# Performance work log

Measured on AMD Instinct MI355X. Metric: run time of the kernel, lower is better.

Reference implementation:

```python
import jax, jax.numpy as jnp
import numpy as np

N_EMBD = 768
HEAD_SIZE = 64
B, T = 8, 4096


def setup_inputs() -> dict:
    key = jax.random.key(0)
    ks = jax.random.split(key, 7)
    s = 0.02  # small init scale for weights
    return {
        "x": jax.random.normal(ks[0], (B, T, N_EMBD), dtype=jnp.float32),
        "Wq": jax.random.normal(ks[1], (N_EMBD, HEAD_SIZE), dtype=jnp.float32) * s,
        "bq": jax.random.normal(ks[2], (HEAD_SIZE,), dtype=jnp.float32) * s,
        "Wk": jax.random.normal(ks[3], (N_EMBD, HEAD_SIZE), dtype=jnp.float32) * s,
        "bk": jax.random.normal(ks[4], (HEAD_SIZE,), dtype=jnp.float32) * s,
        "Wv": jax.random.normal(ks[5], (N_EMBD, HEAD_SIZE), dtype=jnp.float32) * s,
        "bv": jax.random.normal(ks[6], (HEAD_SIZE,), dtype=jnp.float32) * s,
    }


def reference(x, Wq, bq, Wk, bk, Wv, bv):
    # x: [B, T, C]; note: scale uses C = n_embd (input dim), per the original code.
    C = x.shape[-1]
    scale = jnp.asarray(C, x.dtype) ** -0.5
    q = x @ Wq + bq  # [B, T, H]
    k = x @ Wk + bk  # [B, T, H]
    v = x @ Wv + bv  # [B, T, H]
    wei = jnp.einsum("bqh,bkh->bqk", q, k) * scale  # [B, T, T]
    att = jax.nn.softmax(wei, axis=-1)
    # dropout p=0.0 (eval mode) -> identity
    out = jnp.einsum("bqk,bkh->bqh", att, v)  # [B, T, H]
    return out
```

## Files before the change

### kernel.cpp

```cpp
#include <hip/hip_runtime.h>
#include <stdint.h>

#define T_SEQ 4096
#define CEMB 768
#define HS 64

typedef __attribute__((ext_vector_type(8))) short bf16x8;
typedef __attribute__((ext_vector_type(16))) float f32x16;

__device__ __forceinline__ short bfru(float f) {
    uint32_t u = __builtin_bit_cast(uint32_t, f);
    return (short)((u + 0x8000u) >> 16);
}
__device__ __forceinline__ short bftr(float f) {
    return (short)(__builtin_bit_cast(uint32_t, f) >> 16);
}

#define QSCALE (0.036084391824351615f * 1.4426950408889634f)

__global__ __launch_bounds__(256) void prep_wt(const float* __restrict__ Wq,
                                               const float* __restrict__ Wk,
                                               const float* __restrict__ Wv,
                                               short* __restrict__ wtf) {
    const int p = blockIdx.x;
    const int ct = p / 48, kq = p % 48;
    const int tid = threadIdx.x;
    const int lane = tid & 63, jp = tid >> 6;
    const int l31 = lane & 31, lhi = lane >> 5;
    const int k = kq * 16 + lhi * 8 + jp * 2;
    const int nn = ct * 32 + l31;
    const float* W = nn < 64 ? Wq : (nn < 128 ? Wk : Wv);
    const int col = nn & 63;
    uint32_t lo = (uint16_t)bfru(W[k * 64 + col]);
    uint32_t hi = (uint16_t)bfru(W[(k + 1) * 64 + col]);
    *(uint32_t*)&wtf[(p * 64 + lane) * 8 + jp * 2] = lo | (hi << 16);
}

__global__ __launch_bounds__(256) void qkv_proj(const float* __restrict__ x,
        const float* __restrict__ bq, const float* __restrict__ bk, const float* __restrict__ bv,
        const short* __restrict__ wtf,
        short* __restrict__ qo, short* __restrict__ ko, short* __restrict__ vto) {
    __shared__ short S[64 * 72];

    const int tid  = threadIdx.x;
    const int wave = tid >> 6, lane = tid & 63;
    const int l31  = lane & 31, lhi = lane >> 5;
    const int rg   = wave & 1;
    const int ctb  = (wave >> 1) * 3;
    const int rowbase = blockIdx.x * 64;

    f32x16 acc[3];
    #pragma unroll
    for (int c = 0; c < 3; ++c) {
        const int ct = ctb + c, nn = ct * 32 + l31;
        const float bb = nn < 64 ? bq[nn] : (nn < 128 ? bk[nn - 64] : bv[nn - 128]);
        #pragma unroll
        for (int r = 0; r < 16; ++r) acc[c][r] = bb;
    }

    const int sr = tid >> 2, sseg = (tid & 3) * 16;
    for (int kt = 0; kt < 12; ++kt) {
        const float4* src = (const float4*)(x + (long)(rowbase + sr) * CEMB + kt * 64 + sseg);
        float4 f0 = src[0], f1 = src[1], f2 = src[2], f3 = src[3];
        bf16x8 w0, w1;
        w0[0]=bfru(f0.x); w0[1]=bfru(f0.y); w0[2]=bfru(f0.z); w0[3]=bfru(f0.w);
        w0[4]=bfru(f1.x); w0[5]=bfru(f1.y); w0[6]=bfru(f1.z); w0[7]=bfru(f1.w);
        w1[0]=bfru(f2.x); w1[1]=bfru(f2.y); w1[2]=bfru(f2.z); w1[3]=bfru(f2.w);
        w1[4]=bfru(f3.x); w1[5]=bfru(f3.y); w1[6]=bfru(f3.z); w1[7]=bfru(f3.w);
        *(bf16x8*)&S[sr * 72 + sseg]     = w0;
        *(bf16x8*)&S[sr * 72 + sseg + 8] = w1;
        __syncthreads();
        #pragma unroll
        for (int kc = 0; kc < 4; ++kc) {
            bf16x8 af = *(const bf16x8*)&S[(rg * 32 + l31) * 72 + kc * 16 + lhi * 8];
            #pragma unroll
            for (int c = 0; c < 3; ++c) {
                bf16x8 wf = *(const bf16x8*)&wtf[((ctb + c) * 48 + kt * 4 + kc) * 512 + lane * 8];
                acc[c] = __builtin_amdgcn_mfma_f32_32x32x16_bf16(af, wf, acc[c], 0, 0, 0);
            }
        }
        __syncthreads();
    }

    #pragma unroll
    for (int c = 0; c < 3; ++c) {
        const int ct = ctb + c;
        if (ct < 2) {
            #pragma unroll
            for (int r = 0; r < 16; ++r) {
                const int row = rg * 32 + (r & 3) + 8 * (r >> 2) + 4 * lhi;
                qo[(long)(rowbase + row) * HS + ct * 32 + l31] = bfru(acc[c][r] * QSCALE);
            }
        } else if (ct < 4) {
            #pragma unroll
            for (int r = 0; r < 16; ++r) {
                const int row = rg * 32 + (r & 3) + 8 * (r >> 2) + 4 * lhi;
                ko[(long)(rowbase + row) * HS + (ct - 2) * 32 + l31] = bfru(acc[c][r]);
            }
        } else {
            #pragma unroll
            for (int r = 0; r < 16; ++r) {
                const int row = rg * 32 + (r & 3) + 8 * (r >> 2) + 4 * lhi;
                S[((ct - 4) * 32 + l31) * 72 + row] = bfru(acc[c][r]);
            }
        }
    }
    __syncthreads();
    if (tid < 128) {
        const int vcol = tid >> 1, hh = tid & 1;
        const int b = rowbase >> 12, t0 = rowbase & 4095;
        short* dst = vto + ((long)b * HS + vcol) * T_SEQ + t0 + hh * 32;
        #pragma unroll
        for (int i = 0; i < 4; ++i)
            *(bf16x8*)(dst + i * 8) = *(const bf16x8*)&S[vcol * 72 + hh * 32 + i * 8];
    }
}

__global__ __launch_bounds__(256, 4) void attn(const short* __restrict__ qm,
        const short* __restrict__ km, const short* __restrict__ vtm,
        float* __restrict__ Op, float* __restrict__ lp, const int ks,
        float* __restrict__ outdirect) {
    __shared__ short Klds[64 * 72];
    __shared__ short Vlds[64 * 72];
    __shared__ short Plds[4][32 * 40];

    const int tid  = threadIdx.x;
    const int wave = tid >> 6, lane = tid & 63;
    const int l31  = lane & 31, lhi = lane >> 5;
    const int idx  = blockIdx.x;
    const int b = idx & 7, s = (idx >> 3) % ks, qt = idx / (8 * ks);
    const int slab = T_SEQ / ks, nkt = slab / 64;

    const short* qb = qm + ((long)b * T_SEQ + qt * 128) * HS;
    const short* kb = km + ((long)b * T_SEQ + s * slab) * HS;
    const short* vb = vtm + (long)b * HS * T_SEQ + s * slab;

    bf16x8 qf[4];
    #pragma unroll
    for (int kc = 0; kc < 4; ++kc)
        qf[kc] = *(const bf16x8*)&qb[(wave * 32 + l31) * HS + kc * 16 + lhi * 8];

    bf16x8 ones;
    #pragma unroll
    for (int j = 0; j < 8; ++j) ones[j] = (short)0x3F80;

    f32x16 oacc[2] = {};
    f32x16 lacc = {};
    short* pw = &Plds[wave][0];

    const int sr = tid >> 2, sc = (tid & 3) * 16;
    for (int kt = 0; kt < nkt; ++kt) {
        const int k0 = kt * 64;
        {   const short* p1 = &kb[(k0 + sr) * HS + sc];
            *(bf16x8*)&Klds[sr * 72 + sc]     = *(const bf16x8*)p1;
            *(bf16x8*)&Klds[sr * 72 + sc + 8] = *(const bf16x8*)(p1 + 8); }
        {   const short* p2 = &vb[sr * T_SEQ + k0 + sc];
            *(bf16x8*)&Vlds[sr * 72 + sc]     = *(const bf16x8*)p2;
            *(bf16x8*)&Vlds[sr * 72 + sc + 8] = *(const bf16x8*)(p2 + 8); }
        __syncthreads();

        #pragma unroll
        for (int ct = 0; ct < 2; ++ct) {
            f32x16 z = {};
            #pragma unroll
            for (int kc = 0; kc < 4; ++kc) {
                bf16x8 kf = *(const bf16x8*)&Klds[(ct * 32 + l31) * 72 + kc * 16 + lhi * 8];
                z = __builtin_amdgcn_mfma_f32_32x32x16_bf16(qf[kc], kf, z, 0, 0, 0);
            }
            #pragma unroll
            for (int r = 0; r < 16; ++r) {
                const int row = (r & 3) + 8 * (r >> 2) + 4 * lhi;
                pw[row * 40 + l31] = bftr(__builtin_amdgcn_exp2f(z[r]));
            }
            #pragma unroll
            for (int kc2 = 0; kc2 < 2; ++kc2) {
                bf16x8 pf = *(const bf16x8*)&pw[l31 * 40 + kc2 * 16 + lhi * 8];
                lacc = __builtin_amdgcn_mfma_f32_32x32x16_bf16(pf, ones, lacc, 0, 0, 0);
                #pragma unroll
                for (int ht = 0; ht < 2; ++ht) {
                    bf16x8 vf = *(const bf16x8*)&Vlds[(ht * 32 + l31) * 72 + ct * 32 + kc2 * 16 + lhi * 8];
                    oacc[ht] = __builtin_amdgcn_mfma_f32_32x32x16_bf16(pf, vf, oacc[ht], 0, 0, 0);
                }
            }
        }
        __syncthreads();
    }

    const long rowg = (long)b * T_SEQ + qt * 128 + wave * 32;
    if (outdirect) {
        float* ob = outdirect + rowg * HS;
        #pragma unroll
        for (int ht = 0; ht < 2; ++ht)
            #pragma unroll
            for (int r = 0; r < 16; ++r) {
                const int row = (r & 3) + 8 * (r >> 2) + 4 * lhi;
                ob[row * HS + ht * 32 + l31] = oacc[ht][r] / lacc[r];
            }
    } else {
        float* op = Op + ((long)s * 32768 + rowg) * HS;
        #pragma unroll
        for (int ht = 0; ht < 2; ++ht)
            #pragma unroll
            for (int r = 0; r < 16; ++r) {
                const int row = (r & 3) + 8 * (r >> 2) + 4 * lhi;
                op[row * HS + ht * 32 + l31] = oacc[ht][r];
            }
        if (l31 == 0) {
            #pragma unroll
            for (int r = 0; r < 16; ++r)
                lp[(long)s * 32768 + rowg + (r & 3) + 8 * (r >> 2) + 4 * lhi] = lacc[r];
        }
    }
}

__global__ __launch_bounds__(256) void combine(const float4* __restrict__ Op,
        const float* __restrict__ lp, float4* __restrict__ out, const int ks) {
    const int idx = blockIdx.x * 256 + threadIdx.x;
    const int row = idx >> 4, h4 = idx & 15;
    float ox = 0.f, oy = 0.f, oz = 0.f, ow = 0.f, l = 0.f;
    for (int s = 0; s < ks; ++s) {
        float4 t = Op[(long)(s * 32768 + row) * 16 + h4];
        ox += t.x; oy += t.y; oz += t.z; ow += t.w;
        l += lp[s * 32768 + row];
    }
    const float inv = 1.0f / l;
    float4 o; o.x = ox * inv; o.y = oy * inv; o.z = oz * inv; o.w = ow * inv;
    out[(long)row * 16 + h4] = o;
}

extern "C" void kernel_launch(void* const* d_in, const int* in_sizes, int n_in,
                              void* d_out, int out_size, void* d_ws, size_t ws_size,
                              hipStream_t stream) {
    const float* x  = (const float*)d_in[0];
    const float* Wq = (const float*)d_in[1];
    const float* bq = (const float*)d_in[2];
    const float* Wk = (const float*)d_in[3];
    const float* bk = (const float*)d_in[4];
    const float* Wv = (const float*)d_in[5];
    const float* bv = (const float*)d_in[6];

    char* ws = (char*)d_ws;
    short* qo  = (short*)(ws);
    short* ko  = (short*)(ws + (4u << 20));
    short* vto = (short*)(ws + (8u << 20));
    short* wtf = (short*)(ws + (12u << 20));
    const size_t opOff = 12582912u + 294912u;
    float* Op = (float*)(ws + opOff);

    const size_t per_s = 8388608u + 131072u;
    int ks = (ws_size >= opOff + 4 * per_s) ? 4
           : (ws_size >= opOff + 2 * per_s) ? 2 : 1;
    float* lp = (float*)(ws + opOff + (size_t)ks * 8388608u);

    prep_wt<<<288, 256, 0, stream>>>(Wq, Wk, Wv, wtf);
    qkv_proj<<<512, 256, 0, stream>>>(x, bq, bk, bv, wtf, qo, ko, vto);
    attn<<<256 * ks, 256, 0, stream>>>(qo, ko, vto, Op, lp, ks,
                                       ks == 1 ? (float*)d_out : nullptr);
    if (ks > 1)
        combine<<<2048, 256, 0, stream>>>((const float4*)Op, lp, (float4*)d_out, ks);
}
```

Measured before the change: 227.6 us.

## Restructure attention to 64 query rows per wave with direct-register K/V loads

The attention kernel now gives each wave 64 query rows (two 32-row tiles) and loads K and V fragments straight from global memory into registers, removing the shared K/V staging and both block barriers. S is computed as K·Q^T so P is stored transposed in LDS. The row sum is accumulated in scalar registers from rounded exp values instead of through an MFMA against a ones vector. The QKV projection reads x directly into MFMA fragments without LDS staging and uses a smaller V-transpose buffer. This trades LDS traffic and syncs for more register pressure (occupancy bound lowered to 2) and duplicated global K/V loads across the waves of a block.

```diff
diff --git a/kernel.cpp b/kernel.cpp
--- a/kernel.cpp
+++ b/kernel.cpp
@@ -12,8 +12,8 @@
     uint32_t u = __builtin_bit_cast(uint32_t, f);
     return (short)((u + 0x8000u) >> 16);
 }
-__device__ __forceinline__ short bftr(float f) {
-    return (short)(__builtin_bit_cast(uint32_t, f) >> 16);
+__device__ __forceinline__ uint32_t pack2(float a, float b) {
+    return (uint32_t)(uint16_t)bfru(a) | ((uint32_t)(uint16_t)bfru(b) << 16);
 }
 
 #define QSCALE (0.036084391824351615f * 1.4426950408889634f)
@@ -36,93 +36,84 @@
     *(uint32_t*)&wtf[(p * 64 + lane) * 8 + jp * 2] = lo | (hi << 16);
 }
 
-__global__ __launch_bounds__(256) void qkv_proj(const float* __restrict__ x,
+__global__ __launch_bounds__(256, 2) void qkv_proj(const float* __restrict__ x,
         const float* __restrict__ bq, const float* __restrict__ bk, const float* __restrict__ bv,
         const short* __restrict__ wtf,
         short* __restrict__ qo, short* __restrict__ ko, short* __restrict__ vto) {
-    __shared__ short S[64 * 72];
+    __shared__ short Vtr[2][64 * 40];
 
     const int tid  = threadIdx.x;
     const int wave = tid >> 6, lane = tid & 63;
     const int l31  = lane & 31, lhi = lane >> 5;
-    const int rg   = wave & 1;
-    const int ctb  = (wave >> 1) * 3;
-    const int rowbase = blockIdx.x * 64;
+    const int rg = wave & 1, cb = wave >> 1;
+    const int row0 = blockIdx.x * 64 + rg * 32;
 
     f32x16 acc[3];
     #pragma unroll
     for (int c = 0; c < 3; ++c) {
-        const int ct = ctb + c, nn = ct * 32 + l31;
+        const int nn = (cb * 3 + c) * 32 + l31;
         const float bb = nn < 64 ? bq[nn] : (nn < 128 ? bk[nn - 64] : bv[nn - 128]);
         #pragma unroll
         for (int r = 0; r < 16; ++r) acc[c][r] = bb;
     }
 
-    const int sr = tid >> 2, sseg = (tid & 3) * 16;
+    const float* xr = x + (long)(row0 + l31) * CEMB;
     for (int kt = 0; kt < 12; ++kt) {
-        const float4* src = (const float4*)(x + (long)(rowbase + sr) * CEMB + kt * 64 + sseg);
-        float4 f0 = src[0], f1 = src[1], f2 = src[2], f3 = src[3];
-        bf16x8 w0, w1;
-        w0[0]=bfru(f0.x); w0[1]=bfru(f0.y); w0[2]=bfru(f0.z); w0[3]=bfru(f0.w);
-        w0[4]=bfru(f1.x); w0[5]=bfru(f1.y); w0[6]=bfru(f1.z); w0[7]=bfru(f1.w);
-        w1[0]=bfru(f2.x); w1[1]=bfru(f2.y); w1[2]=bfru(f2.z); w1[3]=bfru(f2.w);
-        w1[4]=bfru(f3.x); w1[5]=bfru(f3.y); w1[6]=bfru(f3.z); w1[7]=bfru(f3.w);
-        *(bf16x8*)&S[sr * 72 + sseg]     = w0;
-        *(bf16x8*)&S[sr * 72 + sseg + 8] = w1;
-        __syncthreads();
         #pragma unroll
         for (int kc = 0; kc < 4; ++kc) {
-            bf16x8 af = *(const bf16x8*)&S[(rg * 32 + l31) * 72 + kc * 16 + lhi * 8];
+            const float* px = xr + kt * 64 + kc * 16 + lhi * 8;
+            float4 a = *(const float4*)px, b2 = *(const float4*)(px + 4);
+            bf16x8 af;
+            af[0]=bfru(a.x);  af[1]=bfru(a.y);  af[2]=bfru(a.z);  af[3]=bfru(a.w);
+            af[4]=bfru(b2.x); af[5]=bfru(b2.y); af[6]=bfru(b2.z); af[7]=bfru(b2.w);
             #pragma unroll
             for (int c = 0; c < 3; ++c) {
-                bf16x8 wf = *(const bf16x8*)&wtf[((ctb + c) * 48 + kt * 4 + kc) * 512 + lane * 8];
+                bf16x8 wf = *(const bf16x8*)&wtf[((cb * 3 + c) * 48 + kt * 4 + kc) * 512 + lane * 8];
                 acc[c] = __builtin_amdgcn_mfma_f32_32x32x16_bf16(af, wf, acc[c], 0, 0, 0);
             }
         }
-        __syncthreads();
     }
 
     #pragma unroll
     for (int c = 0; c < 3; ++c) {
-        const int ct = ctb + c;
+        const int ct = cb * 3 + c;
         if (ct < 2) {
             #pragma unroll
             for (int r = 0; r < 16; ++r) {
-                const int row = rg * 32 + (r & 3) + 8 * (r >> 2) + 4 * lhi;
-                qo[(long)(rowbase + row) * HS + ct * 32 + l31] = bfru(acc[c][r] * QSCALE);
+                const int row = (r & 3) + 8 * (r >> 2) + 4 * lhi;
+                qo[(long)(row0 + row) * HS + ct * 32 + l31] = bfru(acc[c][r] * QSCALE);
             }
         } else if (ct < 4) {
             #pragma unroll
             for (int r = 0; r < 16; ++r) {
-                const int row = rg * 32 + (r & 3) + 8 * (r >> 2) + 4 * lhi;
-                ko[(long)(rowbase + row) * HS + (ct - 2) * 32 + l31] = bfru(acc[c][r]);
+                const int row = (r & 3) + 8 * (r >> 2) + 4 * lhi;
+                ko[(long)(row0 + row) * HS + (ct - 2) * 32 + l31] = bfru(acc[c][r]);
             }
         } else {
-            #pragma unroll
-            for (int r = 0; r < 16; ++r) {
-                const int row = rg * 32 + (r & 3) + 8 * (r >> 2) + 4 * lhi;
-                S[((ct - 4) * 32 + l31) * 72 + row] = bfru(acc[c][r]);
-            }
-        }
-    }
-    __syncthreads();
-    if (tid < 128) {
-        const int vcol = tid >> 1, hh = tid & 1;
-        const int b = rowbase >> 12, t0 = rowbase & 4095;
-        short* dst = vto + ((long)b * HS + vcol) * T_SEQ + t0 + hh * 32;
+            const int vcol = (ct - 4) * 32 + l31;
+            #pragma unroll
+            for (int quad = 0; quad < 4; ++quad) {
+                uint32_t lo = pack2(acc[c][quad * 4 + 0], acc[c][quad * 4 + 1]);
+                uint32_t hi = pack2(acc[c][quad * 4 + 2], acc[c][quad * 4 + 3]);
+                uint32_t* dst = (uint32_t*)&Vtr[rg][vcol * 40 + quad * 8 + lhi * 4];
+                dst[0] = lo; dst[1] = hi;
+            }
+        }
+    }
+    if (cb == 1) {
+        const int b = row0 >> 12, t0 = row0 & 4095;
+        short* dst = vto + ((long)b * HS + lane) * T_SEQ + t0;
         #pragma unroll
         for (int i = 0; i < 4; ++i)
-            *(bf16x8*)(dst + i * 8) = *(const bf16x8*)&S[vcol * 72 + hh * 32 + i * 8];
-    }
-}
-
-__global__ __launch_bounds__(256, 4) void attn(const short* __restrict__ qm,
+            *(bf16x8*)(dst + i * 8) = *(const bf16x8*)&Vtr[rg][lane * 40 + i * 8];
+    }
+}
+
+__global__ __launch_bounds__(256, 2) void attn(const short* __restrict__ qm,
         const short* __restrict__ km, const short* __restrict__ vtm,
         float* __restrict__ Op, float* __restrict__ lp, const int ks,
         float* __restrict__ outdirect) {
-    __shared__ short Klds[64 * 72];
-    __shared__ short Vlds[64 * 72];
-    __shared__ short Plds[4][32 * 40];
+    __shared__ short P[4][2][32 * 72];
 
     const int tid  = threadIdx.x;
     const int wave = tid >> 6, lane = tid & 63;
@@ -130,85 +121,102 @@
     const int idx  = blockIdx.x;
     const int b = idx & 7, s = (idx >> 3) % ks, qt = idx / (8 * ks);
     const int slab = T_SEQ / ks, nkt = slab / 64;
-
-    const short* qb = qm + ((long)b * T_SEQ + qt * 128) * HS;
+    const int qrow0 = qt * 256 + wave * 64;
+
+    const short* qb = qm + ((long)b * T_SEQ + qrow0) * HS;
     const short* kb = km + ((long)b * T_SEQ + s * slab) * HS;
     const short* vb = vtm + (long)b * HS * T_SEQ + s * slab;
 
-    bf16x8 qf[4];
+    bf16x8 qf[2][4];
     #pragma unroll
-    for (int kc = 0; kc < 4; ++kc)
-        qf[kc] = *(const bf16x8*)&qb[(wave * 32 + l31) * HS + kc * 16 + lhi * 8];
-
-    bf16x8 ones;
-    #pragma unroll
-    for (int j = 0; j < 8; ++j) ones[j] = (short)0x3F80;
-
-    f32x16 oacc[2] = {};
-    f32x16 lacc = {};
-    short* pw = &Plds[wave][0];
-
-    const int sr = tid >> 2, sc = (tid & 3) * 16;
+    for (int q = 0; q < 2; ++q)
+        #pragma unroll
+        for (int kc = 0; kc < 4; ++kc)
+            qf[q][kc] = *(const bf16x8*)&qb[(q * 32 + l31) * HS + kc * 16 + lhi * 8];
+
+    f32x16 oacc[2][2] = {};
+    float lsum[2] = {0.f, 0.f};
+    short* pw[2] = { &P[wave][0][0], &P[wave][1][0] };
+
     for (int kt = 0; kt < nkt; ++kt) {
         const int k0 = kt * 64;
-        {   const short* p1 = &kb[(k0 + sr) * HS + sc];
-            *(bf16x8*)&Klds[sr * 72 + sc]     = *(const bf16x8*)p1;
-            *(bf16x8*)&Klds[sr * 72 + sc + 8] = *(const bf16x8*)(p1 + 8); }
-        {   const short* p2 = &vb[sr * T_SEQ + k0 + sc];
-            *(bf16x8*)&Vlds[sr * 72 + sc]     = *(const bf16x8*)p2;
-            *(bf16x8*)&Vlds[sr * 72 + sc + 8] = *(const bf16x8*)(p2 + 8); }
-        __syncthreads();
-
-        #pragma unroll
-        for (int ct = 0; ct < 2; ++ct) {
-            f32x16 z = {};
-            #pragma unroll
-            for (int kc = 0; kc < 4; ++kc) {
-                bf16x8 kf = *(const bf16x8*)&Klds[(ct * 32 + l31) * 72 + kc * 16 + lhi * 8];
-                z = __builtin_amdgcn_mfma_f32_32x32x16_bf16(qf[kc], kf, z, 0, 0, 0);
-            }
-            #pragma unroll
-            for (int r = 0; r < 16; ++r) {
-                const int row = (r & 3) + 8 * (r >> 2) + 4 * lhi;
-                pw[row * 40 + l31] = bftr(__builtin_amdgcn_exp2f(z[r]));
-            }
-            #pragma unroll
-            for (int kc2 = 0; kc2 < 2; ++kc2) {
-                bf16x8 pf = *(const bf16x8*)&pw[l31 * 40 + kc2 * 16 + lhi * 8];
-                lacc = __builtin_amdgcn_mfma_f32_32x32x16_bf16(pf, ones, lacc, 0, 0, 0);
-                #pragma unroll
-                for (int ht = 0; ht < 2; ++ht) {
-                    bf16x8 vf = *(const bf16x8*)&Vlds[(ht * 32 + l31) * 72 + ct * 32 + kc2 * 16 + lhi * 8];
-                    oacc[ht] = __builtin_amdgcn_mfma_f32_32x32x16_bf16(pf, vf, oacc[ht], 0, 0, 0);
+        bf16x8 kf[2][4];
+        #pragma unroll
+        for (int m = 0; m < 2; ++m)
+            #pragma unroll
+            for (int kc = 0; kc < 4; ++kc)
+                kf[m][kc] = *(const bf16x8*)&kb[(k0 + m * 32 + l31) * HS + kc * 16 + lhi * 8];
+        bf16x8 vf[2][4];
+        #pragma unroll
+        for (int ht = 0; ht < 2; ++ht)
+            #pragma unroll
+            for (int kc2 = 0; kc2 < 4; ++kc2)
+                vf[ht][kc2] = *(const bf16x8*)&vb[(ht * 32 + l31) * T_SEQ + k0 + kc2 * 16 + lhi * 8];
+
+        #pragma unroll
+        for (int m = 0; m < 2; ++m) {
+            #pragma unroll
+            for (int q = 0; q < 2; ++q) {
+                f32x16 z = {};
+                #pragma unroll
+                for (int kc = 0; kc < 4; ++kc)
+                    z = __builtin_amdgcn_mfma_f32_32x32x16_bf16(kf[m][kc], qf[q][kc], z, 0, 0, 0);
+                #pragma unroll
+                for (int quad = 0; quad < 4; ++quad) {
+                    uint32_t u0 = (__builtin_bit_cast(uint32_t, __builtin_amdgcn_exp2f(z[quad * 4 + 0])) + 0x8000u) & 0xFFFF0000u;
+                    uint32_t u1 = (__builtin_bit_cast(uint32_t, __builtin_amdgcn_exp2f(z[quad * 4 + 1])) + 0x8000u) & 0xFFFF0000u;
+                    uint32_t u2 = (__builtin_bit_cast(uint32_t, __builtin_amdgcn_exp2f(z[quad * 4 + 2])) + 0x8000u) & 0xFFFF0000u;
+                    uint32_t u3 = (__builtin_bit_cast(uint32_t, __builtin_amdgcn_exp2f(z[quad * 4 + 3])) + 0x8000u) & 0xFFFF0000u;
+                    lsum[q] += (__builtin_bit_cast(float, u0) + __builtin_bit_cast(float, u1))
+                             + (__builtin_bit_cast(float, u2) + __builtin_bit_cast(float, u3));
+                    uint32_t* dst = (uint32_t*)&pw[q][l31 * 72 + m * 32 + quad * 8 + lhi * 4];
+                    dst[0] = (u0 >> 16) | u1;
+                    dst[1] = (u2 >> 16) | u3;
                 }
             }
         }
-        __syncthreads();
-    }
-
-    const long rowg = (long)b * T_SEQ + qt * 128 + wave * 32;
+        #pragma unroll
+        for (int kc2 = 0; kc2 < 4; ++kc2) {
+            bf16x8 pf0 = *(const bf16x8*)&pw[0][l31 * 72 + kc2 * 16 + lhi * 8];
+            bf16x8 pf1 = *(const bf16x8*)&pw[1][l31 * 72 + kc2 * 16 + lhi * 8];
+            #pragma unroll
+            for (int ht = 0; ht < 2; ++ht) {
+                oacc[ht][0] = __builtin_amdgcn_mfma_f32_32x32x16_bf16(vf[ht][kc2], pf0, oacc[ht][0], 0, 0, 0);
+                oacc[ht][1] = __builtin_amdgcn_mfma_f32_32x32x16_bf16(vf[ht][kc2], pf1, oacc[ht][1], 0, 0, 0);
+            }
+        }
+    }
+
+    lsum[0] += __shfl_xor(lsum[0], 32, 64);
+    lsum[1] += __shfl_xor(lsum[1], 32, 64);
+
+    const long rowg = (long)b * T_SEQ + qrow0;
     if (outdirect) {
         float* ob = outdirect + rowg * HS;
         #pragma unroll
-        for (int ht = 0; ht < 2; ++ht)
-            #pragma unroll
-            for (int r = 0; r < 16; ++r) {
-                const int row = (r & 3) + 8 * (r >> 2) + 4 * lhi;
-                ob[row * HS + ht * 32 + l31] = oacc[ht][r] / lacc[r];
-            }
+        for (int q = 0; q < 2; ++q) {
+            const float inv = 1.0f / lsum[q];
+            #pragma unroll
+            for (int ht = 0; ht < 2; ++ht)
+                #pragma unroll
+                for (int r = 0; r < 16; ++r) {
+                    const int h = (r & 3) + 8 * (r >> 2) + 4 * lhi + 32 * ht;
+                    ob[(long)(q * 32 + l31) * HS + h] = oacc[ht][q][r] * inv;
+                }
+        }
     } else {
         float* op = Op + ((long)s * 32768 + rowg) * HS;
         #pragma unroll
-        for (int ht = 0; ht < 2; ++ht)
-            #pragma unroll
-            for (int r = 0; r < 16; ++r) {
-                const int row = (r & 3) + 8 * (r >> 2) + 4 * lhi;
-                op[row * HS + ht * 32 + l31] = oacc[ht][r];
-            }
-        if (l31 == 0) {
-            #pragma unroll
-            for (int r = 0; r < 16; ++r)
-                lp[(long)s * 32768 + rowg + (r & 3) + 8 * (r >> 2) + 4 * lhi] = lacc[r];
+        for (int q = 0; q < 2; ++q) {
+            #pragma unroll
+            for (int ht = 0; ht < 2; ++ht)
+                #pragma unroll
+                for (int r = 0; r < 16; ++r) {
+                    const int h = (r & 3) + 8 * (r >> 2) + 4 * lhi + 32 * ht;
+                    op[(long)(q * 32 + l31) * HS + h] = oacc[ht][q][r];
+                }
+            if (lhi == 0)
+                lp[(long)s * 32768 + rowg + q * 32 + l31] = lsum[q];
         }
     }
 }
@@ -254,8 +262,8 @@
 
     prep_wt<<<288, 256, 0, stream>>>(Wq, Wk, Wv, wtf);
     qkv_proj<<<512, 256, 0, stream>>>(x, bq, bk, bv, wtf, qo, ko, vto);
-    attn<<<256 * ks, 256, 0, stream>>>(qo, ko, vto, Op, lp, ks,
-                                       ks == 1 ? (float*)d_out : nullptr);
+    attn<<<8 * ks * 16, 256, 0, stream>>>(qo, ko, vto, Op, lp, ks,
+                                          ks == 1 ? (float*)d_out : nullptr);
     if (ks > 1)
         combine<<<2048, 256, 0, stream>>>((const float4*)Op, lp, (float4*)d_out, ks);
 }
```

New measurement: 282.1 us. +23.9%, slower.
